# Kernel optimization log

Measured on AMD Instinct MI355X. Metric: run time of the kernel, lower is better.

The kernel has to match this reference:

```python
import jax, jax.numpy as jnp
import numpy as np

COMMITMENT_COST = 0.25


def setup_inputs() -> dict:
    key = jax.random.key(0)
    k1, k2 = jax.random.split(key)
    B, S, D, K = 64, 512, 512, 4096
    inputs = jax.random.normal(k1, (B, S, D), dtype=jnp.float32)
    # codebook initialized uniform(-1/K, 1/K) like the torch module
    codebook = jax.random.uniform(k2, (K, D), dtype=jnp.float32,
                                  minval=-1.0 / K, maxval=1.0 / K)
    return {"inputs": inputs, "codebook": codebook}


def reference(inputs, codebook):
    D = inputs.shape[-1]
    flat = inputs.reshape(-1, D)  # [N, D]
    # squared euclidean distances to every code: [N, K]
    dist = (jnp.sum(flat * flat, axis=1, keepdims=True)
            + jnp.sum(codebook * codebook, axis=1)
            - 2.0 * flat @ codebook.T)
    idx = jnp.argmin(dist, axis=1)  # [N]
    # gather replaces one-hot scatter + matmul (same math)
    quantized = codebook[idx].reshape(inputs.shape)
    commitment_loss = jnp.mean((jax.lax.stop_gradient(quantized) - inputs) ** 2)
    codebook_loss = jnp.mean((quantized - jax.lax.stop_gradient(inputs)) ** 2)
    quantize_loss = COMMITMENT_COST * commitment_loss + codebook_loss
    # straight-through estimator
    quantized_st = inputs + jax.lax.stop_gradient(quantized - inputs)
    encoding_indices = idx.reshape(inputs.shape[:-1])
    return quantized_st, quantize_loss, encoding_indices
```

## Files before the change

### kernel.cpp

```cpp
#include <hip/hip_runtime.h>

#define N_ROWS 32768
#define DIM    512
#define KCODES 4096
#define NPARTS 8
#define KPART  (KCODES / NPARTS)
#define Q_ELEMS (N_ROWS * DIM)
#define LOSS_OFF Q_ELEMS
#define IDX_OFF (Q_ELEMS + 1)

__global__ void k_init(unsigned long long* __restrict__ bk) {
    int i = blockIdx.x * blockDim.x + threadIdx.x;
    if (i < N_ROWS) bk[i] = 0xFFFFFFFFFFFFFFFFull;
}

__global__ void k_cnorm(const float* __restrict__ cb, float* __restrict__ cnorm) {
    int wave = (blockIdx.x * blockDim.x + threadIdx.x) >> 6;
    int lane = threadIdx.x & 63;
    if (wave >= KCODES) return;
    const float4* row = (const float4*)(cb + (size_t)wave * DIM);
    float4 v1 = row[lane];
    float4 v2 = row[lane + 64];
    float s = v1.x*v1.x + v1.y*v1.y + v1.z*v1.z + v1.w*v1.w
            + v2.x*v2.x + v2.y*v2.y + v2.z*v2.z + v2.w*v2.w;
    #pragma unroll
    for (int m = 32; m >= 1; m >>= 1) s += __shfl_xor(s, m);
    if (lane == 0) cnorm[wave] = s;
}

__global__ void k_xnorm(const float* __restrict__ x, float* __restrict__ xnorm) {
    int wave = (blockIdx.x * blockDim.x + threadIdx.x) >> 6;
    int lane = threadIdx.x & 63;
    if (wave >= N_ROWS) return;
    const float4* row = (const float4*)(x + (size_t)wave * DIM);
    float4 v1 = row[lane];
    float4 v2 = row[lane + 64];
    float s = v1.x*v1.x + v1.y*v1.y + v1.z*v1.z + v1.w*v1.w
            + v2.x*v2.x + v2.y*v2.y + v2.z*v2.z + v2.w*v2.w;
    #pragma unroll
    for (int m = 32; m >= 1; m >>= 1) s += __shfl_xor(s, m);
    if (lane == 0) xnorm[wave] = s;
}

#define BM 128
#define BN 128
#define BD 32
#define NTHR 256
#define NCH ((KPART / BN) * (DIM / BD))

__global__ __launch_bounds__(NTHR)
void k_argmin(const float* __restrict__ x, const float* __restrict__ cb,
              const float* __restrict__ cnorm, const float* __restrict__ xnorm,
              unsigned long long* __restrict__ bestkey) {
    __shared__ float xs[BM][BD + 4];
    __shared__ float cs[BD][BN];

    const int tid = threadIdx.x;
    const int ty = tid >> 4;
    const int tx = tid & 15;
    const int r0 = blockIdx.x * BM;
    const int kbase = blockIdx.y * KPART;

    const int ck   = tid & 127;
    const int cdq0 = tid >> 7;

    float xn[8];
    #pragma unroll
    for (int i = 0; i < 8; ++i) xn[i] = xnorm[r0 + ty + 16 * i];

    float best[8];
    int   bidx[8];
    #pragma unroll
    for (int i = 0; i < 8; ++i) { best[i] = 3.4e38f; bidx[i] = kbase; }

    float acc[8][8];

    #pragma unroll 1
    for (int it = 0; it < NCH; ++it) {
        const int kc = it >> 4;
        const int dc = (it & 15) * BD;

        __syncthreads();
        #pragma unroll
        for (int s = 0; s < 4; ++s) {
            int f = tid + s * NTHR;
            int row = f >> 3;
            int dq  = f & 7;
            *(float4*)&xs[row][dq * 4] =
                *(const float4*)(x + (size_t)(r0 + row) * DIM + dc + dq * 4);
        }
        #pragma unroll
        for (int it2 = 0; it2 < 4; ++it2) {
            int dq = cdq0 + it2 * 2;
            float4 v = *(const float4*)(cb + (size_t)(kbase + kc * BN + ck) * DIM + dc + dq * 4);
            cs[dq * 4 + 0][ck] = v.x;
            cs[dq * 4 + 1][ck] = v.y;
            cs[dq * 4 + 2][ck] = v.z;
            cs[dq * 4 + 3][ck] = v.w;
        }
        __syncthreads();

        if ((it & 15) == 0) {
            #pragma unroll
            for (int i = 0; i < 8; ++i)
                #pragma unroll
                for (int j = 0; j < 8; ++j) acc[i][j] = 0.f;
        }

        #pragma unroll
        for (int d4 = 0; d4 < 8; ++d4) {
            float4 xa[8];
            #pragma unroll
            for (int i = 0; i < 8; ++i)
                xa[i] = *(const float4*)&xs[ty + 16 * i][d4 * 4];
            #pragma unroll
            for (int dd = 0; dd < 4; ++dd) {
                int d = d4 * 4 + dd;
                float4 b0 = *(const float4*)&cs[d][tx * 4];
                float4 b1 = *(const float4*)&cs[d][64 + tx * 4];
                #pragma unroll
                for (int i = 0; i < 8; ++i) {
                    float a = (dd == 0) ? xa[i].x : (dd == 1) ? xa[i].y
                            : (dd == 2) ? xa[i].z : xa[i].w;
                    acc[i][0] = fmaf(a, b0.x, acc[i][0]);
                    acc[i][1] = fmaf(a, b0.y, acc[i][1]);
                    acc[i][2] = fmaf(a, b0.z, acc[i][2]);
                    acc[i][3] = fmaf(a, b0.w, acc[i][3]);
                    acc[i][4] = fmaf(a, b1.x, acc[i][4]);
                    acc[i][5] = fmaf(a, b1.y, acc[i][5]);
                    acc[i][6] = fmaf(a, b1.z, acc[i][6]);
                    acc[i][7] = fmaf(a, b1.w, acc[i][7]);
                }
            }
        }

        if ((it & 15) == 15) {
            #pragma unroll
            for (int half = 0; half < 2; ++half) {
                #pragma unroll
                for (int j = 0; j < 4; ++j) {
                    int k = kbase + kc * BN + half * 64 + tx * 4 + j;
                    float cn = cnorm[k];
                    #pragma unroll
                    for (int i = 0; i < 8; ++i) {
                        float t1 = xn[i] + cn;
                        float tw = 2.0f * acc[i][half * 4 + j];
                        float s  = t1 - tw;
                        if (s < best[i]) { best[i] = s; bidx[i] = k; }
                    }
                }
            }
        }
    }

    #pragma unroll
    for (int i = 0; i < 8; ++i) {
        float b = best[i];
        int   ix = bidx[i];
        #pragma unroll
        for (int m = 1; m <= 8; m <<= 1) {
            float ob = __shfl_xor(b, m);
            int   oi = __shfl_xor(ix, m);
            if (ob < b || (ob == b && oi < ix)) { b = ob; ix = oi; }
        }
        if (tx == 0) {
            int row = r0 + ty + 16 * i;
            unsigned int ub = __float_as_uint(b);
            ub = (ub & 0x80000000u) ? ~ub : (ub | 0x80000000u);
            unsigned long long key = ((unsigned long long)ub << 32) | (unsigned int)ix;
            atomicMin(bestkey + row, key);
        }
    }
}

__global__ void k_gather(const float* __restrict__ x, const float* __restrict__ cb,
                         const unsigned long long* __restrict__ bestkey,
                         float* __restrict__ qout, float* __restrict__ idx_out,
                         float* __restrict__ partial) {
    int row  = blockIdx.x * 4 + (threadIdx.x >> 6);
    int lane = threadIdx.x & 63;
    int bk = (int)(bestkey[row] & 0xFFFFFFFFull);
    if (lane == 0) idx_out[row] = (float)bk;
    const float4* crow = (const float4*)(cb + (size_t)bk * DIM);
    const float4* xrow = (const float4*)(x + (size_t)row * DIM);
    float4* qrow = (float4*)(qout + (size_t)row * DIM);
    float s = 0.f;
    #pragma unroll
    for (int it = 0; it < 2; ++it) {
        int d4 = lane + it * 64;
        float4 q = crow[d4];
        float4 xi = xrow[d4];
        qrow[d4] = q;
        float dx = q.x - xi.x; s += dx * dx;
        dx = q.y - xi.y; s += dx * dx;
        dx = q.z - xi.z; s += dx * dx;
        dx = q.w - xi.w; s += dx * dx;
    }
    #pragma unroll
    for (int m = 32; m >= 1; m >>= 1) s += __shfl_xor(s, m);
    __shared__ float ws4[4];
    if (lane == 0) ws4[threadIdx.x >> 6] = s;
    __syncthreads();
    if (threadIdx.x == 0)
        partial[blockIdx.x] = (ws4[0] + ws4[1]) + (ws4[2] + ws4[3]);
}

__global__ void k_loss(const float* __restrict__ partial, float* __restrict__ out_loss) {
    int t = threadIdx.x;
    double s = 0.0;
    #pragma unroll 4
    for (int i = 0; i < 32; ++i) s += (double)partial[t * 32 + i];
    #pragma unroll
    for (int m = 32; m >= 1; m >>= 1) s += __shfl_xor(s, m);
    __shared__ double sd[4];
    if ((t & 63) == 0) sd[t >> 6] = s;
    __syncthreads();
    if (t == 0) {
        double tot = (sd[0] + sd[1]) + (sd[2] + sd[3]);
        out_loss[0] = (float)(1.25 * tot / (double)Q_ELEMS);
    }
}

extern "C" void kernel_launch(void* const* d_in, const int* in_sizes, int n_in,
                              void* d_out, int out_size, void* d_ws, size_t ws_size,
                              hipStream_t stream) {
    const float* x  = (const float*)d_in[0];
    const float* cb = (const float*)d_in[1];
    float* out = (float*)d_out;

    char* ws = (char*)d_ws;
    unsigned long long* bestkey = (unsigned long long*)ws;  ws += (size_t)N_ROWS * 8;
    float* cnorm = (float*)ws;                              ws += (size_t)KCODES * 4;
    float* xnorm = (float*)ws;                              ws += (size_t)N_ROWS * 4;
    float* part  = (float*)ws;

    k_init<<<N_ROWS / 256, 256, 0, stream>>>(bestkey);
    k_cnorm<<<KCODES / 4, 256, 0, stream>>>(cb, cnorm);
    k_xnorm<<<N_ROWS / 4, 256, 0, stream>>>(x, xnorm);
    dim3 agrid(N_ROWS / BM, NPARTS);
    k_argmin<<<agrid, NTHR, 0, stream>>>(x, cb, cnorm, xnorm, bestkey);
    k_gather<<<N_ROWS / 4, 256, 0, stream>>>(x, cb, bestkey, out, out + IDX_OFF, part);
    k_loss<<<1, 256, 0, stream>>>(part, out + LOSS_OFF);
}
```

Before: 1.701 ms.

## Double-buffer argmin tiles via direct global-to-LDS loads with XOR swizzle

Replaces the register-staged, transposed LDS fills in the distance/argmin GEMM with global_load_lds direct copies into a double buffer, so the next tile is fetched while the current one is computed. Both the input and codebook tiles are stored row-major with an XOR swizzle on the float4 column so the compute loop can read them without bank conflicts. The codebook is now read as float4 along D per column instead of from a transposed layout. This removes one barrier per iteration and the VGPR round-trip for loads, but relies on the wave-level LDS layout and swizzle being exactly right, and doubles LDS use.

```diff
diff --git a/kernel.cpp b/kernel.cpp
--- a/kernel.cpp
+++ b/kernel.cpp
@@ -1,4 +1,5 @@
 #include <hip/hip_runtime.h>
+#include <stdint.h>
 
 #define N_ROWS 32768
 #define DIM    512
@@ -8,6 +9,10 @@
 #define Q_ELEMS (N_ROWS * DIM)
 #define LOSS_OFF Q_ELEMS
 #define IDX_OFF (Q_ELEMS + 1)
+
+#define GLL(g, l) __builtin_amdgcn_global_load_lds( \
+    (const __attribute__((address_space(1))) void*)(g), \
+    (__attribute__((address_space(3))) void*)(l), 16, 0, 0)
 
 __global__ void k_init(unsigned long long* __restrict__ bk) {
     int i = blockIdx.x * blockDim.x + threadIdx.x;
@@ -52,8 +57,7 @@
 void k_argmin(const float* __restrict__ x, const float* __restrict__ cb,
               const float* __restrict__ cnorm, const float* __restrict__ xnorm,
               unsigned long long* __restrict__ bestkey) {
-    __shared__ float xs[BM][BD + 4];
-    __shared__ float cs[BD][BN];
+    __shared__ float smem[2 * 2 * 4096];
 
     const int tid = threadIdx.x;
     const int ty = tid >> 4;
@@ -61,8 +65,18 @@
     const int r0 = blockIdx.x * BM;
     const int kbase = blockIdx.y * KPART;
 
-    const int ck   = tid & 127;
-    const int cdq0 = tid >> 7;
+    const float* gx[4];
+    const float* gc[4];
+    #pragma unroll
+    for (int s = 0; s < 4; ++s) {
+        int p   = s * 256 + tid;
+        int row = p >> 3;
+        int d4x = (tid & 7) ^ (row & 7);
+        gx[s] = x + (size_t)(r0 + row) * DIM + d4x * 4;
+        int d4c = (tid & 7) ^ ((row >> 2) & 7);
+        gc[s] = cb + (size_t)(kbase + row) * DIM + d4c * 4;
+    }
+    const int w = __builtin_amdgcn_readfirstlane(tid >> 6);
 
     float xn[8];
     #pragma unroll
@@ -75,30 +89,30 @@
 
     float acc[8][8];
 
+    auto STAGE = [&](int it, int b) {
+        const int kc  = it >> 4;
+        const int dcf = (it & 15) * BD;
+        const size_t coff = (size_t)kc * (BN * DIM) + dcf;
+        char* lb = (char*)smem + b * 32768;
+        #pragma unroll
+        for (int s = 0; s < 4; ++s) {
+            GLL(gx[s] + dcf,  lb + s * 4096 + w * 1024);
+            GLL(gc[s] + coff, lb + 16384 + s * 4096 + w * 1024);
+        }
+    };
+
+    STAGE(0, 0);
+    __syncthreads();
+
+    const int tym = ty & 7;
+    const int txm = tx & 7;
+
     #pragma unroll 1
     for (int it = 0; it < NCH; ++it) {
+        const int b  = it & 1;
         const int kc = it >> 4;
-        const int dc = (it & 15) * BD;
-
-        __syncthreads();
-        #pragma unroll
-        for (int s = 0; s < 4; ++s) {
-            int f = tid + s * NTHR;
-            int row = f >> 3;
-            int dq  = f & 7;
-            *(float4*)&xs[row][dq * 4] =
-                *(const float4*)(x + (size_t)(r0 + row) * DIM + dc + dq * 4);
-        }
-        #pragma unroll
-        for (int it2 = 0; it2 < 4; ++it2) {
-            int dq = cdq0 + it2 * 2;
-            float4 v = *(const float4*)(cb + (size_t)(kbase + kc * BN + ck) * DIM + dc + dq * 4);
-            cs[dq * 4 + 0][ck] = v.x;
-            cs[dq * 4 + 1][ck] = v.y;
-            cs[dq * 4 + 2][ck] = v.z;
-            cs[dq * 4 + 3][ck] = v.w;
-        }
-        __syncthreads();
+
+        if (it + 1 < NCH) STAGE(it + 1, b ^ 1);
 
         if ((it & 15) == 0) {
             #pragma unroll
@@ -106,30 +120,39 @@
                 #pragma unroll
                 for (int j = 0; j < 8; ++j) acc[i][j] = 0.f;
         }
+
+        const float* xbuf = smem + b * 8192;
+        const float* cbuf = smem + b * 8192 + 4096;
 
         #pragma unroll
         for (int d4 = 0; d4 < 8; ++d4) {
             float4 xa[8];
+            const int xoff = (d4 ^ tym) * 4;
             #pragma unroll
             for (int i = 0; i < 8; ++i)
-                xa[i] = *(const float4*)&xs[ty + 16 * i][d4 * 4];
-            #pragma unroll
-            for (int dd = 0; dd < 4; ++dd) {
-                int d = d4 * 4 + dd;
-                float4 b0 = *(const float4*)&cs[d][tx * 4];
-                float4 b1 = *(const float4*)&cs[d][64 + tx * 4];
-                #pragma unroll
-                for (int i = 0; i < 8; ++i) {
-                    float a = (dd == 0) ? xa[i].x : (dd == 1) ? xa[i].y
-                            : (dd == 2) ? xa[i].z : xa[i].w;
-                    acc[i][0] = fmaf(a, b0.x, acc[i][0]);
-                    acc[i][1] = fmaf(a, b0.y, acc[i][1]);
-                    acc[i][2] = fmaf(a, b0.z, acc[i][2]);
-                    acc[i][3] = fmaf(a, b0.w, acc[i][3]);
-                    acc[i][4] = fmaf(a, b1.x, acc[i][4]);
-                    acc[i][5] = fmaf(a, b1.y, acc[i][5]);
-                    acc[i][6] = fmaf(a, b1.z, acc[i][6]);
-                    acc[i][7] = fmaf(a, b1.w, acc[i][7]);
+                xa[i] = *(const float4*)(xbuf + (ty + 16 * i) * 32 + xoff);
+            const int coffd = (d4 ^ txm) * 4;
+            #pragma unroll
+            for (int jh = 0; jh < 2; ++jh) {
+                float4 cv[4];
+                #pragma unroll
+                for (int jj = 0; jj < 4; ++jj) {
+                    int col = jh * 64 + tx * 4 + jj;
+                    cv[jj] = *(const float4*)(cbuf + col * 32 + coffd);
+                }
+                #pragma unroll
+                for (int dd = 0; dd < 4; ++dd) {
+                    #pragma unroll
+                    for (int i = 0; i < 8; ++i) {
+                        float a = (dd == 0) ? xa[i].x : (dd == 1) ? xa[i].y
+                                : (dd == 2) ? xa[i].z : xa[i].w;
+                        #pragma unroll
+                        for (int jj = 0; jj < 4; ++jj) {
+                            float bv = (dd == 0) ? cv[jj].x : (dd == 1) ? cv[jj].y
+                                     : (dd == 2) ? cv[jj].z : cv[jj].w;
+                            acc[i][jh * 4 + jj] = fmaf(a, bv, acc[i][jh * 4 + jj]);
+                        }
+                    }
                 }
             }
         }
@@ -151,6 +174,8 @@
                 }
             }
         }
+
+        __syncthreads();
     }
 
     #pragma unroll
```

Result: slower. 2.048 ms (+20.4%).
